# Kernel tuning notes

Hardware: AMD Instinct MI355X
Metric: run time of the kernel (lower is better)

## Reference

```python
import jax, jax.numpy as jnp
import numpy as np

S = 1.0 / np.sqrt(2.0).astype(np.float32)  # Haar normalization


def _dwt_axis(x, axis):
    """Level-1 Haar DWT along `axis` (length must be even).
    Returns (lo, hi), each half-length along axis."""
    x = jnp.moveaxis(x, axis, -1)
    n = x.shape[-1]
    xp = x.reshape(x.shape[:-1] + (n // 2, 2))
    lo = (xp[..., 0] + xp[..., 1]) * S
    hi = (xp[..., 0] - xp[..., 1]) * S
    return jnp.moveaxis(lo, -1, axis), jnp.moveaxis(hi, -1, axis)


def _idwt_axis(lo, hi, axis, orig_len):
    """Inverse level-1 Haar along `axis`: interleave (lo+hi)*s, (lo-hi)*s."""
    lo = jnp.moveaxis(lo, axis, -1)
    hi = jnp.moveaxis(hi, axis, -1)
    even = (lo + hi) * S
    odd = (lo - hi) * S
    rec = jnp.stack([even, odd], axis=-1).reshape(lo.shape[:-1] + (2 * lo.shape[-1],))
    rec = rec[..., :orig_len]
    return jnp.moveaxis(rec, -1, axis)


def _mix(sub, W, b):
    # 1x1 conv = channel mixing: (B,C,H,W), W: (Cout,Cin), b: (Cout,)
    return jnp.einsum('oc,bchw->bohw', W, sub) + b[None, :, None, None]


def setup_inputs() -> dict:
    key = jax.random.key(0)
    B, C, H, W = 8, 64, 256, 256
    ks = jax.random.split(key, 9)
    scale = 1.0 / C
    inp = {'x': jax.random.normal(ks[0], (B, C, H, W), dtype=jnp.float32)}
    for i, name in enumerate(['LL', 'LH', 'HL', 'HH']):
        inp[f'w_{name}'] = jax.random.uniform(ks[1 + i], (C, C), jnp.float32, -scale, scale)
        inp[f'b_{name}'] = jnp.zeros((C,), jnp.float32)
    return inp


def reference(x, w_LL, b_LL, w_LH, b_LH, w_HL, b_HL, w_HH, b_HH):
    B, C, H, W = x.shape
    # DWT: along W then along H (separable Haar)
    Lw, Hw = _dwt_axis(x, -1)
    LL, LH = _dwt_axis(Lw, -2)
    HL, HH = _dwt_axis(Hw, -2)
    # Per-subband 1x1 channel mixers
    LL = _mix(LL, w_LL, b_LL)
    LH = _mix(LH, w_LH, b_LH)
    HL = _mix(HL, w_HL, b_HL)
    HH = _mix(HH, w_HH, b_HH)
    # IDWT: along H then along W
    Lw_r = _idwt_axis(LL, LH, -2, H)
    Hw_r = _idwt_axis(HL, HH, -2, H)
    return _idwt_axis(Lw_r, Hw_r, -1, W)
```

## Files before the change

### kernel.cpp

```cpp
#include <hip/hip_runtime.h>
#include <hip/hip_bf16.h>


using bf16x8 = __attribute__((ext_vector_type(8))) short;
using f32x4  = __attribute__((ext_vector_type(4))) float;

__device__ inline unsigned short f2bf(float v) {
    __hip_bfloat16 h = __float2bfloat16(v);
    return __builtin_bit_cast(unsigned short, h);
}

__global__ __launch_bounds__(256) void wvc_prep(
    const float* __restrict__ wLL, const float* __restrict__ bLL,
    const float* __restrict__ wLH, const float* __restrict__ bLH,
    const float* __restrict__ wHL, const float* __restrict__ bHL,
    const float* __restrict__ wHH, const float* __restrict__ bHH,
    unsigned short* __restrict__ afrag, float* __restrict__ bcomb)
{
    const int idx  = blockIdx.x * 256 + threadIdx.x;
    const int i    = idx & 7;
    const int lane = (idx >> 3) & 63;
    const int mt   = (idx >> 9) & 3;
    const int ks   = (idx >> 11) & 1;
    const int band = (idx >> 12) & 3;
    const float* Ws[4] = {wLL, wLH, wHL, wHH};
    const int o = mt * 16 + (lane & 15);
    const int c = ks * 32 + (lane >> 4) * 8 + i;
    afrag[idx] = f2bf(0.5f * Ws[band][o * 64 + c]);

    if (blockIdx.x == 0 && threadIdx.x < 64) {
        const int t = threadIdx.x;
        float b0 = bLL[t], b1 = bLH[t], b2 = bHL[t], b3 = bHH[t];
        bcomb[0 * 64 + t] = 0.5f * (b0 + b1 + b2 + b3);
        bcomb[1 * 64 + t] = 0.5f * (b0 + b1 - b2 - b3);
        bcomb[2 * 64 + t] = 0.5f * (b0 - b1 + b2 - b3);
        bcomb[3 * 64 + t] = 0.5f * (b0 - b1 - b2 + b3);
    }
}

#define NT 8
__global__ __launch_bounds__(512, 2) void wvc_main(
    const float* __restrict__ x,
    const unsigned short* __restrict__ afrag_g,
    const float* __restrict__ bcomb,
    float* __restrict__ out)
{
    __shared__ __align__(16) unsigned char lds_x[2][65792];
    __shared__ __align__(16) float lds_bc[256];

    const int tid = threadIdx.x;
    const int l   = tid & 63;
    const int wv  = tid >> 6;
    const int blk = blockIdx.x;
    const int b   = blk >> 5;
    const int jt  = (blk >> 4) & 1;
    const int ig  = blk & 15;
    const int w0  = jt * 128;

    const int sg   = wv & 3;
    const int m0   = (wv >> 2) * 2;
    const int site = sg * 16 + (l & 15);
    const int lg   = l >> 4;

    if (tid < 256) lds_bc[tid] = bcomb[tid];

    const unsigned short* afb = afrag_g + (size_t)l * 8;
    bf16x8 a[4][2][2];
    #pragma unroll
    for (int bd = 0; bd < 4; ++bd)
        #pragma unroll
        for (int ks = 0; ks < 2; ++ks)
            #pragma unroll
            for (int mtl = 0; mtl < 2; ++mtl)
                a[bd][ks][mtl] = *(const bf16x8*)(
                    afb + (size_t)((bd * 2 + ks) * 4 + m0 + mtl) * 512);

    const float* xb = x + (size_t)b * 4194304 + (size_t)(wv * 8) * 65536
                        + (size_t)(l >> 5) * 256 + w0 + (l & 31) * 4;
    unsigned char* lb[2] = { &lds_x[0][wv * 8 * 1024 + wv * 32],
                             &lds_x[1][wv * 8 * 1024 + wv * 32] };

    {
        const float* g = xb + (size_t)(ig * 8 + 0) * 512;
        #pragma unroll
        for (int k = 0; k < 8; ++k)
            __builtin_amdgcn_global_load_lds(
                (const __attribute__((address_space(1))) void*)(g + (size_t)k * 65536),
                (__attribute__((address_space(3))) void*)(lb[0] + k * 1024),
                16, 0, 0);
    }
    asm volatile("s_waitcnt lgkmcnt(0)" ::: "memory");

    for (int t = 0; t < NT; ++t) {
        if (t + 1 < NT) {
            const float* g = xb + (size_t)(ig * 8 + t + 1) * 512;
            unsigned char* lbn = lb[(t + 1) & 1];
            #pragma unroll
            for (int k = 0; k < 8; ++k)
                __builtin_amdgcn_global_load_lds(
                    (const __attribute__((address_space(1))) void*)(g + (size_t)k * 65536),
                    (__attribute__((address_space(3))) void*)(lbn + k * 1024),
                    16, 0, 0);
            asm volatile("s_waitcnt vmcnt(8)" ::: "memory");
        } else {
            asm volatile("s_waitcnt vmcnt(0)" ::: "memory");
        }
        __builtin_amdgcn_sched_barrier(0);
        __builtin_amdgcn_s_barrier();
        __builtin_amdgcn_sched_barrier(0);

        const unsigned char* bx = lds_x[t & 1];

        bf16x8 bfr[4][2];
        #pragma unroll
        for (int ks = 0; ks < 2; ++ks) {
            float2 p0[8], p1[8];
            #pragma unroll
            for (int i = 0; i < 8; ++i) {
                const int ch = ks * 32 + lg * 8 + i;
                const unsigned char* base =
                    bx + ch * 1024 + (ks * 4 + lg) * 32 + site * 8;
                p0[i] = *(const float2*)(base);
                p1[i] = *(const float2*)(base + 512);
            }
            #pragma unroll
            for (int i = 0; i < 8; ++i) {
                float aa = p0[i].x + p0[i].y, mm = p0[i].x - p0[i].y;
                float cc = p1[i].x + p1[i].y, dd = p1[i].x - p1[i].y;
                bfr[0][ks][i] = (short)f2bf(aa + cc);
                bfr[1][ks][i] = (short)f2bf(aa - cc);
                bfr[2][ks][i] = (short)f2bf(mm + dd);
                bfr[3][ks][i] = (short)f2bf(mm - dd);
            }
        }

        f32x4 acc[4][2];
        #pragma unroll
        for (int bd = 0; bd < 4; ++bd)
            #pragma unroll
            for (int mtl = 0; mtl < 2; ++mtl)
                acc[bd][mtl] = (f32x4){0.f, 0.f, 0.f, 0.f};
        #pragma unroll
        for (int bd = 0; bd < 4; ++bd)
            #pragma unroll
            for (int ks = 0; ks < 2; ++ks)
                #pragma unroll
                for (int mtl = 0; mtl < 2; ++mtl)
                    acc[bd][mtl] = __builtin_amdgcn_mfma_f32_16x16x32_bf16(
                        a[bd][ks][mtl], bfr[bd][ks], acc[bd][mtl], 0, 0, 0);

        const int h0 = (ig * 8 + t) * 2;
        float* ob = out + (size_t)b * 4194304 + (size_t)h0 * 256 + w0 + 2 * site;
        #pragma unroll
        for (int mtl = 0; mtl < 2; ++mtl) {
            const int ob0 = (m0 + mtl) * 16 + lg * 4;
            f32x4 bc0 = *(const f32x4*)(&lds_bc[  0 + ob0]);
            f32x4 bc1 = *(const f32x4*)(&lds_bc[ 64 + ob0]);
            f32x4 bc2 = *(const f32x4*)(&lds_bc[128 + ob0]);
            f32x4 bc3 = *(const f32x4*)(&lds_bc[192 + ob0]);
            #pragma unroll
            for (int r = 0; r < 4; ++r) {
                float y0 = acc[0][mtl][r];
                float y1 = acc[1][mtl][r];
                float y2 = acc[2][mtl][r];
                float y3 = acc[3][mtl][r];
                float s01 = y0 + y1, d01 = y0 - y1;
                float s23 = y2 + y3, d23 = y2 - y3;
                float e00 = 0.5f * (s01 + s23) + bc0[r];
                float e01 = 0.5f * (s01 - s23) + bc1[r];
                float e10 = 0.5f * (d01 + d23) + bc2[r];
                float e11 = 0.5f * (d01 - d23) + bc3[r];
                float* po = ob + (size_t)(ob0 + r) * 65536;
                float2 v0; v0.x = e00; v0.y = e01;
                float2 v1; v1.x = e10; v1.y = e11;
                *(float2*)po         = v0;
                *(float2*)(po + 256) = v1;
            }
        }

        __builtin_amdgcn_sched_barrier(0);
        __builtin_amdgcn_s_barrier();
        __builtin_amdgcn_sched_barrier(0);
    }
}

extern "C" void kernel_launch(void* const* d_in, const int* in_sizes, int n_in,
                              void* d_out, int out_size, void* d_ws, size_t ws_size,
                              hipStream_t stream) {
    const float* x   = (const float*)d_in[0];
    const float* wLL = (const float*)d_in[1];
    const float* bLL = (const float*)d_in[2];
    const float* wLH = (const float*)d_in[3];
    const float* bLH = (const float*)d_in[4];
    const float* wHL = (const float*)d_in[5];
    const float* bHL = (const float*)d_in[6];
    const float* wHH = (const float*)d_in[7];
    const float* bHH = (const float*)d_in[8];
    float* out = (float*)d_out;

    unsigned short* afrag = (unsigned short*)d_ws;
    float* bcomb = (float*)((char*)d_ws + 32768);

    wvc_prep<<<64, 256, 0, stream>>>(wLL, bLL, wLH, bLH, wHL, bHL, wHH, bHH,
                                     afrag, bcomb);
    wvc_main<<<256, 512, 0, stream>>>(x, afrag, bcomb, out);
}
```

Baseline: 55.78 us.

## Halve block width tile to 64 columns and let output stores stay in flight

Each block now uses 256 threads and a 64-column tile instead of 512 threads and 128 columns. That doubles the grid to 512 blocks, halves the double-buffered LDS footprint and reshapes the per-channel LDS rows to 512 bytes with adjusted padding. The vmcnt waits are recomputed so the 16 output stores from the previous iteration no longer have to drain before the next tile's loads are consumed. The aim is better latency hiding and more blocks resident per CU on a kernel that is close to bandwidth-bound. The cost is hand-tuned wait counts that depend on how many stores the compiler emits, which makes the synchronisation more fragile.

```diff
diff --git a/kernel.cpp b/kernel.cpp
--- a/kernel.cpp
+++ b/kernel.cpp
@@ -39,30 +39,30 @@
 }
 
 #define NT 8
-__global__ __launch_bounds__(512, 2) void wvc_main(
+__global__ __launch_bounds__(256, 2) void wvc_main(
     const float* __restrict__ x,
     const unsigned short* __restrict__ afrag_g,
     const float* __restrict__ bcomb,
     float* __restrict__ out)
 {
-    __shared__ __align__(16) unsigned char lds_x[2][65792];
+    __shared__ __align__(64) unsigned char lds_x[2][33024];
     __shared__ __align__(16) float lds_bc[256];
 
     const int tid = threadIdx.x;
     const int l   = tid & 63;
     const int wv  = tid >> 6;
     const int blk = blockIdx.x;
-    const int b   = blk >> 5;
-    const int jt  = (blk >> 4) & 1;
+    const int b   = blk >> 6;
+    const int jq  = (blk >> 4) & 3;
     const int ig  = blk & 15;
-    const int w0  = jt * 128;
-
-    const int sg   = wv & 3;
-    const int m0   = (wv >> 2) * 2;
+    const int w0  = jq * 64;
+
+    const int sg   = wv & 1;
+    const int m0   = (wv >> 1) * 2;
     const int site = sg * 16 + (l & 15);
     const int lg   = l >> 4;
 
-    if (tid < 256) lds_bc[tid] = bcomb[tid];
+    lds_bc[tid] = bcomb[tid];
 
     const unsigned short* afb = afrag_g + (size_t)l * 8;
     bf16x8 a[4][2][2];
@@ -75,18 +75,19 @@
                 a[bd][ks][mtl] = *(const bf16x8*)(
                     afb + (size_t)((bd * 2 + ks) * 4 + m0 + mtl) * 512);
 
-    const float* xb = x + (size_t)b * 4194304 + (size_t)(wv * 8) * 65536
-                        + (size_t)(l >> 5) * 256 + w0 + (l & 31) * 4;
-    unsigned char* lb[2] = { &lds_x[0][wv * 8 * 1024 + wv * 32],
-                             &lds_x[1][wv * 8 * 1024 + wv * 32] };
+    const float* xb = x + (size_t)b * 4194304
+                        + (size_t)(wv * 16 + (l >> 5)) * 65536
+                        + (size_t)((l >> 4) & 1) * 256 + w0 + (l & 15) * 4;
+    const int lbo = (wv * 16) * 512 + (wv * 2) * 32;
 
     {
         const float* g = xb + (size_t)(ig * 8 + 0) * 512;
+        unsigned char* lbn = &lds_x[0][lbo];
         #pragma unroll
         for (int k = 0; k < 8; ++k)
             __builtin_amdgcn_global_load_lds(
-                (const __attribute__((address_space(1))) void*)(g + (size_t)k * 65536),
-                (__attribute__((address_space(3))) void*)(lb[0] + k * 1024),
+                (const __attribute__((address_space(1))) void*)(g + (size_t)(2 * k) * 65536),
+                (__attribute__((address_space(3))) void*)(lbn + k * 1024 + (k >> 2) * 32),
                 16, 0, 0);
     }
     asm volatile("s_waitcnt lgkmcnt(0)" ::: "memory");
@@ -94,17 +95,17 @@
     for (int t = 0; t < NT; ++t) {
         if (t + 1 < NT) {
             const float* g = xb + (size_t)(ig * 8 + t + 1) * 512;
-            unsigned char* lbn = lb[(t + 1) & 1];
+            unsigned char* lbn = &lds_x[(t + 1) & 1][lbo];
             #pragma unroll
             for (int k = 0; k < 8; ++k)
                 __builtin_amdgcn_global_load_lds(
-                    (const __attribute__((address_space(1))) void*)(g + (size_t)k * 65536),
-                    (__attribute__((address_space(3))) void*)(lbn + k * 1024),
+                    (const __attribute__((address_space(1))) void*)(g + (size_t)(2 * k) * 65536),
+                    (__attribute__((address_space(3))) void*)(lbn + k * 1024 + (k >> 2) * 32),
                     16, 0, 0);
-            asm volatile("s_waitcnt vmcnt(8)" ::: "memory");
-        } else {
-            asm volatile("s_waitcnt vmcnt(0)" ::: "memory");
         }
+        if (t == 0)            asm volatile("s_waitcnt vmcnt(8)"  ::: "memory");
+        else if (t + 1 < NT)   asm volatile("s_waitcnt vmcnt(24)" ::: "memory");
+        else                   asm volatile("s_waitcnt vmcnt(16)" ::: "memory");
         __builtin_amdgcn_sched_barrier(0);
         __builtin_amdgcn_s_barrier();
         __builtin_amdgcn_sched_barrier(0);
@@ -117,11 +118,11 @@
             float2 p0[8], p1[8];
             #pragma unroll
             for (int i = 0; i < 8; ++i) {
-                const int ch = ks * 32 + lg * 8 + i;
                 const unsigned char* base =
-                    bx + ch * 1024 + (ks * 4 + lg) * 32 + site * 8;
+                    bx + (size_t)(ks * 32 + lg * 8 + i) * 512
+                       + (ks * 4 + lg) * 32 + site * 8;
                 p0[i] = *(const float2*)(base);
-                p1[i] = *(const float2*)(base + 512);
+                p1[i] = *(const float2*)(base + 256);
             }
             #pragma unroll
             for (int i = 0; i < 8; ++i) {
@@ -203,5 +204,5 @@
 
     wvc_prep<<<64, 256, 0, stream>>>(wLL, bLL, wLH, bLH, wHL, bHL, wHH, bHH,
                                      afrag, bcomb);
-    wvc_main<<<256, 512, 0, stream>>>(x, afrag, bcomb, out);
-}
+    wvc_main<<<512, 256, 0, stream>>>(x, afrag, bcomb, out);
+}
```

After: 54.83 us. No clear change (-1.7%).
